# Kernel tuning notes

Hardware: AMD Instinct MI355X
Metric: run time of the kernel (lower is better)

The kernel has to match this reference:

```python
import jax, jax.numpy as jnp
import numpy as np

B, S, E, H = 4, 2048, 1024, 16
D = E // H  # head_dim = 64


def setup_inputs() -> dict:
    key = jax.random.key(0)
    ks = jax.random.split(key, 9)
    s = 1.0 / np.sqrt(E)
    return {
        "x": jax.random.normal(ks[0], (B, S, E), dtype=jnp.float32),
        "mask": jnp.ones((B, S), dtype=jnp.int32),
        "Wq": jax.random.uniform(ks[1], (E, E), jnp.float32, -s, s),
        "bq": jnp.zeros((E,), jnp.float32),
        "Wk": jax.random.uniform(ks[2], (E, E), jnp.float32, -s, s),
        "bk": jnp.zeros((E,), jnp.float32),
        "Wv": jax.random.uniform(ks[3], (E, E), jnp.float32, -s, s),
        "bv": jnp.zeros((E,), jnp.float32),
        "Wo": jax.random.uniform(ks[4], (E, E), jnp.float32, -s, s),
        "bo": jnp.zeros((E,), jnp.float32),
    }


def reference(x, mask, Wq, bq, Wk, bk, Wv, bv, Wo, bo):
    # projections: weights stored as (in, out)
    q = x @ Wq + bq  # [B,S,E]
    k = x @ Wk + bk
    v = x @ Wv + bv
    # split heads: b s (h d) -> b h s d
    q = q.reshape(B, S, H, D).transpose(0, 2, 1, 3)
    k = k.reshape(B, S, H, D).transpose(0, 2, 1, 3)
    v = v.reshape(B, S, H, D).transpose(0, 2, 1, 3)
    scale = 1.0 / np.sqrt(D).astype(np.float32)
    dot = jnp.einsum('bhsd,bhtd->bhst', q, k) * scale  # [B,H,S,S]
    # key padding mask: 1 = valid, 0 = masked
    neg_inf = jnp.asarray(-jnp.inf, dot.dtype)
    dot = jnp.where(mask[:, None, None, :] == 0, neg_inf, dot)
    attn = jax.nn.softmax(dot, axis=-1)
    o = jnp.einsum('bhst,bhtd->bhsd', attn, v)  # [B,H,S,D]
    o = o.transpose(0, 2, 1, 3).reshape(B, S, E)  # merge heads
    return o @ Wo + bo
```

## Files before the change

### kernel.cpp

```cpp
#include <hip/hip_runtime.h>

#define Bc 4
#define Sc 2048
#define Ec 1024
#define Hc 16
#define Dc 64
#define BSc 8192
#define KVB 64

typedef short bf16x8 __attribute__((ext_vector_type(8)));
typedef float f32x4 __attribute__((ext_vector_type(4)));
typedef unsigned short u16;
typedef unsigned long long u64;

__device__ __forceinline__ u16 f2bf(float f){
  unsigned u = __builtin_bit_cast(unsigned, f);
  u += 0x7FFFu + ((u >> 16) & 1u);
  return (u16)(u >> 16);
}
__device__ __forceinline__ void gll16(const void* g, void* l){
  __builtin_amdgcn_global_load_lds((const __attribute__((address_space(1))) void*)g,
                                   (__attribute__((address_space(3))) void*)l, 16, 0, 0);
}
__device__ __forceinline__ float exp2_s(float x){
#if __has_builtin(__builtin_amdgcn_exp2f)
  return __builtin_amdgcn_exp2f(x);
#else
  return exp2f(x);
#endif
}
__device__ __forceinline__ unsigned cvtpk(float a, float b){
  unsigned r;
  asm volatile("v_cvt_pk_bf16_f32 %0, %1, %2\n\ts_nop 1" : "=v"(r) : "v"(a), "v"(b));
  return r;
}

__global__ void cvt_x_kernel(const float* __restrict__ x, u16* __restrict__ xb, int n){
  int i = (blockIdx.x * 256 + threadIdx.x) * 4;
  if (i >= n) return;
  float4 v = *(const float4*)(x + i);
  *(ushort4*)(xb+i) = make_ushort4(f2bf(v.x), f2bf(v.y), f2bf(v.z), f2bf(v.w));
}

__global__ void wt_kernel(const float* __restrict__ w0, const float* __restrict__ w1,
                          const float* __restrict__ w2, const float* __restrict__ w3,
                          u16* __restrict__ wt){
  const float* w = blockIdx.z==0 ? w0 : blockIdx.z==1 ? w1 : blockIdx.z==2 ? w2 : w3;
  u16* ho = wt + (size_t)blockIdx.z * Ec * Ec;
  __shared__ float t[32][33];
  int k0 = blockIdx.y * 32, n0 = blockIdx.x * 32;
  int tx = threadIdx.x & 31, ty = threadIdx.x >> 5;
  for (int i = 0; i < 4; ++i){
    int k = ty + i*8;
    t[k][tx] = w[(size_t)(k0+k)*Ec + n0 + tx];
  }
  __syncthreads();
  for (int i = 0; i < 4; ++i){
    int nn = ty + i*8;
    ho[(size_t)(n0+nn)*Ec + k0 + tx] = f2bf(t[tx][nn]);
  }
}

__global__ __launch_bounds__(256, 2)
void gemm_qkv(const u16* __restrict__ A, const u16* __restrict__ Wt,
              const float* __restrict__ bq, const float* __restrict__ bk,
              const float* __restrict__ bv,
              u16* __restrict__ qout, u16* __restrict__ kout, u16* __restrict__ vout)
{
  constexpr int K = Ec;
  __shared__ alignas(16) u16 As[128*32];
  __shared__ alignas(16) u16 Bs[128*32];
  const int tid = threadIdx.x, lane = tid & 63, w = tid >> 6;
  const int wr = w >> 1, wc = w & 1;
  const int m0 = blockIdx.y * 128;
  const int n0g = blockIdx.x * 128;
  const int which = n0g >> 10;
  const int n0 = n0g & 1023;
  const u16* Bt = Wt + (size_t)which * Ec * Ec;
  const float* bias = which == 0 ? bq : which == 1 ? bk : bv;
  const int l15 = lane & 15, kslot = lane >> 4;
  const f32x4 fz = {0.f,0.f,0.f,0.f};
  f32x4 acc[4][4];
  for (int i=0;i<4;++i) for (int j=0;j<4;++j) acc[i][j] = fz;

  const int srow = lane >> 2, sslot = lane & 3;

  for (int k0 = 0; k0 < K; k0 += 32){
    __syncthreads();
    for (int i = 0; i < 2; ++i){
      int c = w*2 + i;
      int row = c*16 + srow;
      int sw = (row ^ (row >> 2)) & 3;
      gll16(A  + (size_t)(m0+row)*K + k0 + ((sslot ^ sw) << 3), As + c*512);
      gll16(Bt + (size_t)(n0+row)*K + k0 + ((sslot ^ sw) << 3), Bs + c*512);
    }
    __syncthreads();
    bf16x8 af[4], bfr[4];
    for (int mi = 0; mi < 4; ++mi){
      int row = wr*64 + mi*16 + l15;
      int sw = (row ^ (row >> 2)) & 3;
      af[mi] = *(const bf16x8*)(As + row*32 + ((kslot ^ sw) << 3));
    }
    for (int ni = 0; ni < 4; ++ni){
      int row = wc*64 + ni*16 + l15;
      int sw = (row ^ (row >> 2)) & 3;
      bfr[ni] = *(const bf16x8*)(Bs + row*32 + ((kslot ^ sw) << 3));
    }
    for (int mi = 0; mi < 4; ++mi)
      for (int ni = 0; ni < 4; ++ni)
        acc[mi][ni] = __builtin_amdgcn_mfma_f32_16x16x32_bf16(af[mi], bfr[ni], acc[mi][ni], 0, 0, 0);
  }

  for (int mi = 0; mi < 4; ++mi){
    for (int ni = 0; ni < 4; ++ni){
      int col = n0 + wc*64 + ni*16 + l15;
      int row0 = m0 + wr*64 + mi*16 + kslot*4;
      float bi = bias[col];
      if (which == 2){
        int bb = row0 >> 11, s0 = row0 & 2047;
        int hh = col >> 6, dd = col & 63;
        ushort4 pk = make_ushort4(f2bf(acc[mi][ni][0]+bi), f2bf(acc[mi][ni][1]+bi),
                                  f2bf(acc[mi][ni][2]+bi), f2bf(acc[mi][ni][3]+bi));
        *(ushort4*)(vout + ((size_t)(bb*Hc+hh)*Dc + dd)*Sc + s0) = pk;
      } else {
        u16* dst = which == 0 ? qout : kout;
        for (int j = 0; j < 4; ++j){
          float v = acc[mi][ni][j] + bi;
          int row = row0 + j;
          float vv = (which == 0) ? v * 0.18033688f : v;
          int bb = row >> 11, ss = row & 2047;
          int hh = col >> 6, dd = col & 63;
          dst[((size_t)(bb*Hc+hh)*Sc + ss)*Dc + dd] = f2bf(vv);
        }
      }
    }
  }
}

__global__ __launch_bounds__(256, 2)
void gemm_out(const u16* __restrict__ A, const u16* __restrict__ Bt,
              const float* __restrict__ bias, float* __restrict__ outp)
{
  constexpr int K = Ec;
  __shared__ alignas(16) u16 As[128*32];
  __shared__ alignas(16) u16 Bs[128*32];
  const int tid = threadIdx.x, lane = tid & 63, w = tid >> 6;
  const int wr = w >> 1, wc = w & 1;
  const int m0 = blockIdx.y * 128, n0 = blockIdx.x * 128;
  const int l15 = lane & 15, kslot = lane >> 4;
  const f32x4 fz = {0.f,0.f,0.f,0.f};
  f32x4 acc[4][4];
  for (int i=0;i<4;++i) for (int j=0;j<4;++j) acc[i][j] = fz;

  const int srow = lane >> 2, sslot = lane & 3;

  for (int k0 = 0; k0 < K; k0 += 32){
    __syncthreads();
    for (int i = 0; i < 2; ++i){
      int c = w*2 + i;
      int row = c*16 + srow;
      int sw = (row ^ (row >> 2)) & 3;
      gll16(A  + (size_t)(m0+row)*K + k0 + ((sslot ^ sw) << 3), As + c*512);
      gll16(Bt + (size_t)(n0+row)*K + k0 + ((sslot ^ sw) << 3), Bs + c*512);
    }
    __syncthreads();
    bf16x8 af[4], bfr[4];
    for (int mi = 0; mi < 4; ++mi){
      int row = wr*64 + mi*16 + l15;
      int sw = (row ^ (row >> 2)) & 3;
      af[mi] = *(const bf16x8*)(As + row*32 + ((kslot ^ sw) << 3));
    }
    for (int ni = 0; ni < 4; ++ni){
      int row = wc*64 + ni*16 + l15;
      int sw = (row ^ (row >> 2)) & 3;
      bfr[ni] = *(const bf16x8*)(Bs + row*32 + ((kslot ^ sw) << 3));
    }
    for (int mi = 0; mi < 4; ++mi)
      for (int ni = 0; ni < 4; ++ni)
        acc[mi][ni] = __builtin_amdgcn_mfma_f32_16x16x32_bf16(af[mi], bfr[ni], acc[mi][ni], 0, 0, 0);
  }

  for (int mi = 0; mi < 4; ++mi){
    for (int ni = 0; ni < 4; ++ni){
      int col = n0 + wc*64 + ni*16 + l15;
      int row0 = m0 + wr*64 + mi*16 + kslot*4;
      float bi = bias[col];
      for (int j = 0; j < 4; ++j)
        outp[(size_t)(row0+j)*Ec + col] = acc[mi][ni][j] + bi;
    }
  }
}

__global__ __launch_bounds__(256, 2)
void attn_kernel(const u16* __restrict__ qb, const u16* __restrict__ kb,
                 const u16* __restrict__ vt, const int* __restrict__ mask,
                 u16* __restrict__ ob)
{
  __shared__ alignas(16) u16 Ks[2][KVB*Dc];
  __shared__ alignas(16) u16 Vs[2][Dc*KVB];
  const int tid = threadIdx.x, lane = tid & 63, w = tid >> 6;
  const int l15 = lane & 15, ks = lane >> 4;
  const int wg = ((blockIdx.x & 7) << 7) | (blockIdx.x >> 3);
  const int bh = wg >> 4, qblk = wg & 15;
  const int b = bh >> 4, h = bh & 15;
  const int q0 = qblk*128 + w*32;

  const u16* Q  = qb + (size_t)bh*Sc*Dc;
  const u16* Kg = kb + (size_t)bh*Sc*Dc;
  const u16* Vg = vt + (size_t)bh*Dc*Sc;
  const int* mpb = mask + b*Sc;

  int nzl = 1;
  {
    const int4* mv4 = (const int4*)mpb;
#pragma unroll
    for (int i = 0; i < 8; ++i){
      int4 v = mv4[i*64 + lane];
      nzl &= (v.x && v.y && v.z && v.w) ? 1 : 0;
    }
  }
  const bool allvalid = __all(nzl);

  int koff[2], voff[2];
#pragma unroll
  for (int i = 0; i < 2; ++i){
    int S = (w*2+i)*64 + lane;
    int row = S >> 3, s = S & 7;
    koff[i] = row*Dc + ((s ^ (row & 7)) << 3);
    voff[i] = row*Sc + ((s ^ (row & 7)) << 3);
  }
  const int Xl = (l15 & 7) << 4;

  bf16x8 qf[2][2];
#pragma unroll
  for (int qa = 0; qa < 2; ++qa)
#pragma unroll
    for (int kd = 0; kd < 2; ++kd)
      qf[qa][kd] = *(const bf16x8*)(Q + (size_t)(q0 + qa*16 + l15)*Dc + kd*32 + ks*8);

  bf16x8 onesb;
#pragma unroll
  for (int j = 0; j < 8; ++j) onesb[j] = (short)0x3F80;

  const f32x4 fz = {0.f,0.f,0.f,0.f};
  f32x4 o[2][4];
#pragma unroll
  for (int qa = 0; qa < 2; ++qa)
#pragma unroll
    for (int db = 0; db < 4; ++db) o[qa][db] = fz;
  float m[2] = {-3e38f, -3e38f}, runl[2] = {0.f, 0.f};

#pragma unroll
  for (int i = 0; i < 2; ++i){
    gll16(Kg + koff[i], &Ks[0][(w*2+i)*512]);
    gll16(Vg + voff[i], &Vs[0][(w*2+i)*512]);
  }

  const int NT = Sc / KVB;
  int cur = 0;
  for (int t = 0; t < NT; ++t){
    asm volatile("s_waitcnt vmcnt(0)" ::: "memory");
    __syncthreads();
    if (t + 1 < NT){
      const u16* kg = Kg + (size_t)(t+1)*(KVB*Dc);
      const u16* vg = Vg + (size_t)(t+1)*KVB;
#pragma unroll
      for (int i = 0; i < 2; ++i){
        gll16(kg + koff[i], &Ks[cur^1][(w*2+i)*512]);
        gll16(vg + voff[i], &Vs[cur^1][(w*2+i)*512]);
      }
    }
    const char* Ksb = (const char*)&Ks[cur][0];
    const char* Vsb = (const char*)&Vs[cur][0];

    f32x4 sc[4][2];
#pragma unroll
    for (int nb = 0; nb < 4; ++nb){
      bf16x8 kf0 = *(const bf16x8*)(Ksb + nb*2048 + l15*128 + (((0*4+ks) << 4) ^ Xl));
      bf16x8 kf1 = *(const bf16x8*)(Ksb + nb*2048 + l15*128 + (((1*4+ks) << 4) ^ Xl));
#pragma unroll
      for (int qa = 0; qa < 2; ++qa){
        sc[nb][qa] = __builtin_amdgcn_mfma_f32_16x16x32_bf16(kf0, qf[qa][0], fz, 0,0,0);
        sc[nb][qa] = __builtin_amdgcn_mfma_f32_16x16x32_bf16(kf1, qf[qa][1], sc[nb][qa], 0,0,0);
      }
    }
    if (!allvalid){
      const int* mp = mpb + t*KVB;
#pragma unroll
      for (int nb = 0; nb < 4; ++nb)
#pragma unroll
        for (int r = 0; r < 4; ++r){
          float bi = mp[nb*16 + ks*4 + r] ? 0.f : -3e38f;
          sc[nb][0][r] += bi;
          sc[nb][1][r] += bi;
        }
    }
    float pmax[2];
#pragma unroll
    for (int qa = 0; qa < 2; ++qa){
      f32x4 mx4;
#pragma unroll
      for (int r = 0; r < 4; ++r)
        mx4[r] = fmaxf(fmaxf(sc[0][qa][r], sc[1][qa][r]),
                       fmaxf(sc[2][qa][r], sc[3][qa][r]));
      pmax[qa] = fmaxf(fmaxf(mx4[0], mx4[1]), fmaxf(mx4[2], mx4[3]));
    }
    int ok = (t > 0) && (pmax[0] <= m[0] + 8.f) && (pmax[1] <= m[1] + 8.f);
    if (!__all(ok)){
#pragma unroll
      for (int qa = 0; qa < 2; ++qa){
        float tv = pmax[qa];
        tv = fmaxf(tv, __shfl_xor(tv, 16, 64));
        tv = fmaxf(tv, __shfl_xor(tv, 32, 64));
        float nm = fmaxf(m[qa], tv);
        float al = exp2_s(m[qa] - nm);
        m[qa] = nm;
        runl[qa] *= al;
#pragma unroll
        for (int db = 0; db < 4; ++db)
#pragma unroll
          for (int r = 0; r < 4; ++r)
            o[qa][db][r] *= al;
      }
    }
#pragma unroll
    for (int nb = 0; nb < 4; ++nb)
#pragma unroll
      for (int qa = 0; qa < 2; ++qa)
#pragma unroll
        for (int r = 0; r < 4; ++r)
          sc[nb][qa][r] = exp2_s(sc[nb][qa][r] - m[qa]);

    f32x4 accl[2] = {fz, fz};
#pragma unroll
    for (int kt = 0; kt < 2; ++kt){
      bf16x8 pb[2];
#pragma unroll
      for (int qa = 0; qa < 2; ++qa){
        union { bf16x8 v; unsigned u[4]; } pu;
        pu.u[0] = cvtpk(sc[2*kt  ][qa][0], sc[2*kt  ][qa][1]);
        pu.u[1] = cvtpk(sc[2*kt  ][qa][2], sc[2*kt  ][qa][3]);
        pu.u[2] = cvtpk(sc[2*kt+1][qa][0], sc[2*kt+1][qa][1]);
        pu.u[3] = cvtpk(sc[2*kt+1][qa][2], sc[2*kt+1][qa][3]);
        pb[qa] = pu.v;
      }
      accl[0] = __builtin_amdgcn_mfma_f32_16x16x32_bf16(onesb, pb[0], accl[0], 0,0,0);
      accl[1] = __builtin_amdgcn_mfma_f32_16x16x32_bf16(onesb, pb[1], accl[1], 0,0,0);
#pragma unroll
      for (int db = 0; db < 4; ++db){
        union { bf16x8 v; u64 q[2]; } vu;
        const int g0 = kt*4 + (ks >> 1);
        const int base = db*2048 + l15*128 + (ks & 1)*8;
        vu.q[0] = *(const u64*)(Vsb + base + (((g0    ) << 4) ^ Xl));
        vu.q[1] = *(const u64*)(Vsb + base + (((g0 + 2) << 4) ^ Xl));
#pragma unroll
        for (int qa = 0; qa < 2; ++qa)
          o[qa][db] = __builtin_amdgcn_mfma_f32_16x16x32_bf16(vu.v, pb[qa], o[qa][db], 0,0,0);
      }
    }
    runl[0] += accl[0][0];
    runl[1] += accl[1][0];
    cur ^= 1;
  }
#pragma unroll
  for (int qa = 0; qa < 2; ++qa){
    float inv = __builtin_amdgcn_rcpf(fmaxf(runl[qa], 1e-35f));
    u16* orow = ob + ((size_t)(b*Sc + q0 + qa*16 + l15))*Ec + h*Dc + ks*4;
#pragma unroll
    for (int db = 0; db < 4; ++db){
      ushort4 pk = make_ushort4(f2bf(o[qa][db][0]*inv), f2bf(o[qa][db][1]*inv),
                                f2bf(o[qa][db][2]*inv), f2bf(o[qa][db][3]*inv));
      *(ushort4*)(orow + db*16) = pk;
    }
  }
}

extern "C" void kernel_launch(void* const* d_in, const int* in_sizes, int n_in,
                              void* d_out, int out_size, void* d_ws, size_t ws_size,
                              hipStream_t stream) {
  const float* x  = (const float*)d_in[0];
  const int* mask = (const int*)d_in[1];
  const float* Wq = (const float*)d_in[2];
  const float* bq = (const float*)d_in[3];
  const float* Wk = (const float*)d_in[4];
  const float* bk = (const float*)d_in[5];
  const float* Wv = (const float*)d_in[6];
  const float* bv = (const float*)d_in[7];
  const float* Wo = (const float*)d_in[8];
  const float* bo = (const float*)d_in[9];
  float* out = (float*)d_out;

  u16* ws   = (u16*)d_ws;
  u16* x_bf = ws;
  u16* w_t  = x_bf + (size_t)BSc*Ec;
  u16* q_bf = w_t  + (size_t)4*Ec*Ec;
  u16* k_bf = q_bf + (size_t)BSc*Ec;
  u16* v_t  = k_bf + (size_t)BSc*Ec;
  u16* o_bf = v_t  + (size_t)BSc*Ec;

  cvt_x_kernel<<<BSc*Ec/1024, 256, 0, stream>>>(x, x_bf, BSc*Ec);
  wt_kernel<<<dim3(32,32,4), 256, 0, stream>>>(Wq, Wk, Wv, Wo, w_t);

  const size_t WSZ = (size_t)Ec*Ec;
  gemm_qkv<<<dim3(24,64), 256, 0, stream>>>(x_bf, w_t, bq, bk, bv, q_bf, k_bf, v_t);

  attn_kernel<<<dim3(1024), 256, 0, stream>>>(q_bf, k_bf, v_t, mask, o_bf);

  gemm_out<<<dim3(8,64), 256, 0, stream>>>(o_bf, w_t+3*WSZ, bo, out);
}
```

Measured before the change: 204.7 us.

## Process two KV tiles per barrier and store Q transposed for vectorized epilogue

The attention loop now stages two 64-key K/V tiles per double-buffer slot, halving the number of waitcnt/syncthreads barriers and issuing larger prefetch batches. Q is written by the projection GEMM in a transposed (d-major) layout using packed ushort4 stores, like V, instead of scattered scalar stores. The attention kernel then gathers Q fragments with strided scalar loads once per wave. Shared memory per block doubles (64KB), which may reduce occupancy below the declared two blocks per CU.

New measurement: 220.6 us. 1.08x slower.

```diff
diff --git a/kernel.cpp b/kernel.cpp
--- a/kernel.cpp
+++ b/kernel.cpp
@@ -116,21 +116,21 @@
       int col = n0 + wc*64 + ni*16 + l15;
       int row0 = m0 + wr*64 + mi*16 + kslot*4;
       float bi = bias[col];
-      if (which == 2){
+      if (which != 1){
         int bb = row0 >> 11, s0 = row0 & 2047;
         int hh = col >> 6, dd = col & 63;
-        ushort4 pk = make_ushort4(f2bf(acc[mi][ni][0]+bi), f2bf(acc[mi][ni][1]+bi),
-                                  f2bf(acc[mi][ni][2]+bi), f2bf(acc[mi][ni][3]+bi));
-        *(ushort4*)(vout + ((size_t)(bb*Hc+hh)*Dc + dd)*Sc + s0) = pk;
+        float sc0 = (which == 0) ? 0.18033688f : 1.0f;
+        u16* dst = (which == 0) ? qout : vout;
+        ushort4 pk = make_ushort4(f2bf((acc[mi][ni][0]+bi)*sc0), f2bf((acc[mi][ni][1]+bi)*sc0),
+                                  f2bf((acc[mi][ni][2]+bi)*sc0), f2bf((acc[mi][ni][3]+bi)*sc0));
+        *(ushort4*)(dst + ((size_t)(bb*Hc+hh)*Dc + dd)*Sc + s0) = pk;
       } else {
-        u16* dst = which == 0 ? qout : kout;
         for (int j = 0; j < 4; ++j){
           float v = acc[mi][ni][j] + bi;
           int row = row0 + j;
-          float vv = (which == 0) ? v * 0.18033688f : v;
           int bb = row >> 11, ss = row & 2047;
           int hh = col >> 6, dd = col & 63;
-          dst[((size_t)(bb*Hc+hh)*Sc + ss)*Dc + dd] = f2bf(vv);
+          kout[((size_t)(bb*Hc+hh)*Sc + ss)*Dc + dd] = f2bf(v);
         }
       }
     }
@@ -196,8 +196,8 @@
                  const u16* __restrict__ vt, const int* __restrict__ mask,
                  u16* __restrict__ ob)
 {
-  __shared__ alignas(16) u16 Ks[2][KVB*Dc];
-  __shared__ alignas(16) u16 Vs[2][Dc*KVB];
+  __shared__ alignas(16) u16 Ks[2][2][KVB*Dc];
+  __shared__ alignas(16) u16 Vs[2][2][Dc*KVB];
   const int tid = threadIdx.x, lane = tid & 63, w = tid >> 6;
   const int l15 = lane & 15, ks = lane >> 4;
   const int wg = ((blockIdx.x & 7) << 7) | (blockIdx.x >> 3);
@@ -205,7 +205,7 @@
   const int b = bh >> 4, h = bh & 15;
   const int q0 = qblk*128 + w*32;
 
-  const u16* Q  = qb + (size_t)bh*Sc*Dc;
+  const u16* Q  = qb + (size_t)bh*Dc*Sc;
   const u16* Kg = kb + (size_t)bh*Sc*Dc;
   const u16* Vg = vt + (size_t)bh*Dc*Sc;
   const int* mpb = mask + b*Sc;
@@ -235,8 +235,13 @@
 #pragma unroll
   for (int qa = 0; qa < 2; ++qa)
 #pragma unroll
-    for (int kd = 0; kd < 2; ++kd)
-      qf[qa][kd] = *(const bf16x8*)(Q + (size_t)(q0 + qa*16 + l15)*Dc + kd*32 + ks*8);
+    for (int kd = 0; kd < 2; ++kd){
+      bf16x8 tq;
+#pragma unroll
+      for (int j = 0; j < 8; ++j)
+        tq[j] = (short)Q[(size_t)(kd*32 + ks*8 + j)*Sc + q0 + qa*16 + l15];
+      qf[qa][kd] = tq;
+    }
 
   bf16x8 onesb;
 #pragma unroll
@@ -251,115 +256,124 @@
   float m[2] = {-3e38f, -3e38f}, runl[2] = {0.f, 0.f};
 
 #pragma unroll
-  for (int i = 0; i < 2; ++i){
-    gll16(Kg + koff[i], &Ks[0][(w*2+i)*512]);
-    gll16(Vg + voff[i], &Vs[0][(w*2+i)*512]);
-  }
-
-  const int NT = Sc / KVB;
+  for (int hh2 = 0; hh2 < 2; ++hh2)
+#pragma unroll
+    for (int i = 0; i < 2; ++i){
+      gll16(Kg + hh2*(KVB*Dc) + koff[i], &Ks[0][hh2][(w*2+i)*512]);
+      gll16(Vg + hh2*KVB      + voff[i], &Vs[0][hh2][(w*2+i)*512]);
+    }
+
+  const int NT2 = Sc / (2*KVB);
   int cur = 0;
-  for (int t = 0; t < NT; ++t){
+  for (int t2 = 0; t2 < NT2; ++t2){
     asm volatile("s_waitcnt vmcnt(0)" ::: "memory");
     __syncthreads();
-    if (t + 1 < NT){
-      const u16* kg = Kg + (size_t)(t+1)*(KVB*Dc);
-      const u16* vg = Vg + (size_t)(t+1)*KVB;
-#pragma unroll
-      for (int i = 0; i < 2; ++i){
-        gll16(kg + koff[i], &Ks[cur^1][(w*2+i)*512]);
-        gll16(vg + voff[i], &Vs[cur^1][(w*2+i)*512]);
-      }
-    }
-    const char* Ksb = (const char*)&Ks[cur][0];
-    const char* Vsb = (const char*)&Vs[cur][0];
-
-    f32x4 sc[4][2];
-#pragma unroll
-    for (int nb = 0; nb < 4; ++nb){
-      bf16x8 kf0 = *(const bf16x8*)(Ksb + nb*2048 + l15*128 + (((0*4+ks) << 4) ^ Xl));
-      bf16x8 kf1 = *(const bf16x8*)(Ksb + nb*2048 + l15*128 + (((1*4+ks) << 4) ^ Xl));
+    if (t2 + 1 < NT2){
+      const u16* kg = Kg + (size_t)(t2+1)*(2*KVB*Dc);
+      const u16* vg = Vg + (size_t)(t2+1)*(2*KVB);
+#pragma unroll
+      for (int hh2 = 0; hh2 < 2; ++hh2)
+#pragma unroll
+        for (int i = 0; i < 2; ++i){
+          gll16(kg + hh2*(KVB*Dc) + koff[i], &Ks[cur^1][hh2][(w*2+i)*512]);
+          gll16(vg + hh2*KVB      + voff[i], &Vs[cur^1][hh2][(w*2+i)*512]);
+        }
+    }
+
+#pragma unroll
+    for (int hf = 0; hf < 2; ++hf){
+      const char* Ksb = (const char*)&Ks[cur][hf][0];
+      const char* Vsb = (const char*)&Vs[cur][hf][0];
+      const int t64 = t2*2 + hf;
+
+      f32x4 sc[4][2];
+#pragma unroll
+      for (int nb = 0; nb < 4; ++nb){
+        bf16x8 kf0 = *(const bf16x8*)(Ksb + nb*2048 + l15*128 + (((0*4+ks) << 4) ^ Xl));
+        bf16x8 kf1 = *(const bf16x8*)(Ksb + nb*2048 + l15*128 + (((1*4+ks) << 4) ^ Xl));
+#pragma unroll
+        for (int qa = 0; qa < 2; ++qa){
+          sc[nb][qa] = __builtin_amdgcn_mfma_f32_16x16x32_bf16(kf0, qf[qa][0], fz, 0,0,0);
+          sc[nb][qa] = __builtin_amdgcn_mfma_f32_16x16x32_bf16(kf1, qf[qa][1], sc[nb][qa], 0,0,0);
+        }
+      }
+      if (!allvalid){
+        const int* mp = mpb + t64*KVB;
+#pragma unroll
+        for (int nb = 0; nb < 4; ++nb)
+#pragma unroll
+          for (int r = 0; r < 4; ++r){
+            float bi = mp[nb*16 + ks*4 + r] ? 0.f : -3e38f;
+            sc[nb][0][r] += bi;
+            sc[nb][1][r] += bi;
+          }
+      }
+      float pmax[2];
 #pragma unroll
       for (int qa = 0; qa < 2; ++qa){
-        sc[nb][qa] = __builtin_amdgcn_mfma_f32_16x16x32_bf16(kf0, qf[qa][0], fz, 0,0,0);
-        sc[nb][qa] = __builtin_amdgcn_mfma_f32_16x16x32_bf16(kf1, qf[qa][1], sc[nb][qa], 0,0,0);
-      }
-    }
-    if (!allvalid){
-      const int* mp = mpb + t*KVB;
+        f32x4 mx4;
+#pragma unroll
+        for (int r = 0; r < 4; ++r)
+          mx4[r] = fmaxf(fmaxf(sc[0][qa][r], sc[1][qa][r]),
+                         fmaxf(sc[2][qa][r], sc[3][qa][r]));
+        pmax[qa] = fmaxf(fmaxf(mx4[0], mx4[1]), fmaxf(mx4[2], mx4[3]));
+      }
+      int ok = (t64 > 0) && (pmax[0] <= m[0] + 8.f) && (pmax[1] <= m[1] + 8.f);
+      if (!__all(ok)){
+#pragma unroll
+        for (int qa = 0; qa < 2; ++qa){
+          float tv = pmax[qa];
+          tv = fmaxf(tv, __shfl_xor(tv, 16, 64));
+          tv = fmaxf(tv, __shfl_xor(tv, 32, 64));
+          float nm = fmaxf(m[qa], tv);
+          float al = exp2_s(m[qa] - nm);
+          m[qa] = nm;
+          runl[qa] *= al;
+#pragma unroll
+          for (int db = 0; db < 4; ++db)
+#pragma unroll
+            for (int r = 0; r < 4; ++r)
+              o[qa][db][r] *= al;
+        }
+      }
 #pragma unroll
       for (int nb = 0; nb < 4; ++nb)
 #pragma unroll
-        for (int r = 0; r < 4; ++r){
-          float bi = mp[nb*16 + ks*4 + r] ? 0.f : -3e38f;
-          sc[nb][0][r] += bi;
-          sc[nb][1][r] += bi;
-        }
-    }
-    float pmax[2];
-#pragma unroll
-    for (int qa = 0; qa < 2; ++qa){
-      f32x4 mx4;
-#pragma unroll
-      for (int r = 0; r < 4; ++r)
-        mx4[r] = fmaxf(fmaxf(sc[0][qa][r], sc[1][qa][r]),
-                       fmaxf(sc[2][qa][r], sc[3][qa][r]));
-      pmax[qa] = fmaxf(fmaxf(mx4[0], mx4[1]), fmaxf(mx4[2], mx4[3]));
-    }
-    int ok = (t > 0) && (pmax[0] <= m[0] + 8.f) && (pmax[1] <= m[1] + 8.f);
-    if (!__all(ok)){
-#pragma unroll
-      for (int qa = 0; qa < 2; ++qa){
-        float tv = pmax[qa];
-        tv = fmaxf(tv, __shfl_xor(tv, 16, 64));
-        tv = fmaxf(tv, __shfl_xor(tv, 32, 64));
-        float nm = fmaxf(m[qa], tv);
-        float al = exp2_s(m[qa] - nm);
-        m[qa] = nm;
-        runl[qa] *= al;
-#pragma unroll
-        for (int db = 0; db < 4; ++db)
+        for (int qa = 0; qa < 2; ++qa)
 #pragma unroll
           for (int r = 0; r < 4; ++r)
-            o[qa][db][r] *= al;
-      }
-    }
-#pragma unroll
-    for (int nb = 0; nb < 4; ++nb)
-#pragma unroll
-      for (int qa = 0; qa < 2; ++qa)
-#pragma unroll
-        for (int r = 0; r < 4; ++r)
-          sc[nb][qa][r] = exp2_s(sc[nb][qa][r] - m[qa]);
-
-    f32x4 accl[2] = {fz, fz};
-#pragma unroll
-    for (int kt = 0; kt < 2; ++kt){
-      bf16x8 pb[2];
-#pragma unroll
-      for (int qa = 0; qa < 2; ++qa){
-        union { bf16x8 v; unsigned u[4]; } pu;
-        pu.u[0] = cvtpk(sc[2*kt  ][qa][0], sc[2*kt  ][qa][1]);
-        pu.u[1] = cvtpk(sc[2*kt  ][qa][2], sc[2*kt  ][qa][3]);
-        pu.u[2] = cvtpk(sc[2*kt+1][qa][0], sc[2*kt+1][qa][1]);
-        pu.u[3] = cvtpk(sc[2*kt+1][qa][2], sc[2*kt+1][qa][3]);
-        pb[qa] = pu.v;
-      }
-      accl[0] = __builtin_amdgcn_mfma_f32_16x16x32_bf16(onesb, pb[0], accl[0], 0,0,0);
-      accl[1] = __builtin_amdgcn_mfma_f32_16x16x32_bf16(onesb, pb[1], accl[1], 0,0,0);
-#pragma unroll
-      for (int db = 0; db < 4; ++db){
-        union { bf16x8 v; u64 q[2]; } vu;
-        const int g0 = kt*4 + (ks >> 1);
-        const int base = db*2048 + l15*128 + (ks & 1)*8;
-        vu.q[0] = *(const u64*)(Vsb + base + (((g0    ) << 4) ^ Xl));
-        vu.q[1] = *(const u64*)(Vsb + base + (((g0 + 2) << 4) ^ Xl));
-#pragma unroll
-        for (int qa = 0; qa < 2; ++qa)
-          o[qa][db] = __builtin_amdgcn_mfma_f32_16x16x32_bf16(vu.v, pb[qa], o[qa][db], 0,0,0);
-      }
-    }
-    runl[0] += accl[0][0];
-    runl[1] += accl[1][0];
+            sc[nb][qa][r] = exp2_s(sc[nb][qa][r] - m[qa]);
+
+      f32x4 accl[2] = {fz, fz};
+#pragma unroll
+      for (int kt = 0; kt < 2; ++kt){
+        bf16x8 pb[2];
+#pragma unroll
+        for (int qa = 0; qa < 2; ++qa){
+          union { bf16x8 v; unsigned u[4]; } pu;
+          pu.u[0] = cvtpk(sc[2*kt  ][qa][0], sc[2*kt  ][qa][1]);
+          pu.u[1] = cvtpk(sc[2*kt  ][qa][2], sc[2*kt  ][qa][3]);
+          pu.u[2] = cvtpk(sc[2*kt+1][qa][0], sc[2*kt+1][qa][1]);
+          pu.u[3] = cvtpk(sc[2*kt+1][qa][2], sc[2*kt+1][qa][3]);
+          pb[qa] = pu.v;
+        }
+        accl[0] = __builtin_amdgcn_mfma_f32_16x16x32_bf16(onesb, pb[0], accl[0], 0,0,0);
+        accl[1] = __builtin_amdgcn_mfma_f32_16x16x32_bf16(onesb, pb[1], accl[1], 0,0,0);
+#pragma unroll
+        for (int db = 0; db < 4; ++db){
+          union { bf16x8 v; u64 q[2]; } vu;
+          const int g0 = kt*4 + (ks >> 1);
+          const int base = db*2048 + l15*128 + (ks & 1)*8;
+          vu.q[0] = *(const u64*)(Vsb + base + (((g0    ) << 4) ^ Xl));
+          vu.q[1] = *(const u64*)(Vsb + base + (((g0 + 2) << 4) ^ Xl));
+#pragma unroll
+          for (int qa = 0; qa < 2; ++qa)
+            o[qa][db] = __builtin_amdgcn_mfma_f32_16x16x32_bf16(vu.v, pb[qa], o[qa][db], 0,0,0);
+        }
+      }
+      runl[0] += accl[0][0];
+      runl[1] += accl[1][0];
+    }
     cur ^= 1;
   }
 #pragma unroll
```
